# Kernel optimization log

Measured on AMD Instinct MI355X. Metric: run time of the kernel, lower is better.

## Reference

```python
import jax, jax.numpy as jnp
import numpy as np

SP = 4          # window/split size
HEADS = 8       # num_heads
SHIFTS = (0, 2) # shift_sizes


def _rel_pos_index(sp):
    # Same construction as the torch buffer `relative_position_index`.
    coords = np.stack(np.meshgrid(np.arange(sp), np.arange(sp), indexing='ij'))  # [2,sp,sp]
    coords = coords.reshape(2, -1)                                               # [2, sp*sp]
    rel = coords[:, :, None] - coords[:, None, :]                                # [2, N, N]
    rel = rel.transpose(1, 2, 0).astype(np.int64)                                # [N, N, 2]
    rel[..., 0] += sp - 1
    rel[..., 1] += sp - 1
    rel[..., 0] *= 2 * sp - 1
    return rel.sum(-1)  # [N, N]


def _window_attend(xh, qkv_w, lepe_w, bias, sp, heads, scale):
    # xh: [B, c, H, W] with c = split_dim
    B, c, H, W = xh.shape
    hd = c // heads
    h, w = H // sp, W // sp
    # 1x1 conv to qkv (no bias)
    qkv = jnp.einsum('oi,bihw->bohw', qkv_w, xh)
    q, k, v = jnp.split(qkv, 3, axis=1)
    # depthwise 3x3 LePE on v
    lepe = jax.lax.conv_general_dilated(v, lepe_w, (1, 1), 'SAME',
                                        feature_group_count=c)

    def part(t):
        # 'b (c head) (h hsp) (w wsp) -> (b h w) head (hsp wsp) c'
        t = t.reshape(B, hd, heads, h, sp, w, sp)
        t = t.transpose(0, 3, 5, 2, 4, 6, 1)  # b,h,w,head,hsp,wsp,hd
        return t.reshape(B * h * w, heads, sp * sp, hd)

    q, k, v, lepe = map(part, (q, k, v, lepe))
    attn = jnp.einsum('nhqc,nhkc->nhqk', q * scale, k) + bias[None]  # [N,heads,16,16]
    attn = jax.nn.softmax(attn, axis=-1)
    out = jnp.einsum('nhqk,nhkc->nhqc', attn, v) + lepe
    # inverse rearrange back to [B, c, H, W]
    out = out.reshape(B, h, w, heads, sp, sp, hd)
    out = out.transpose(0, 6, 3, 1, 4, 2, 5).reshape(B, c, H, W)
    return out


def setup_inputs() -> dict:
    key = jax.random.key(0)
    k1, k2, k3, k4 = jax.random.split(key, 4)
    x = jax.random.normal(k1, (8, 128, 192, 192), dtype=jnp.float32)
    qkv_w = jax.random.normal(k2, (192, 64), dtype=jnp.float32) * 0.05   # [3*split_dim, split_dim]
    lepe_w = jax.random.normal(k3, (64, 1, 3, 3), dtype=jnp.float32) * 0.05  # depthwise
    bias_table = jax.random.normal(k4, (49, 8), dtype=jnp.float32) * 0.02    # [(2sp-1)^2, heads]
    return {'x': x, 'qkv_w': qkv_w, 'lepe_w': lepe_w, 'bias_table': bias_table}


def reference(x, qkv_w, lepe_w, bias_table):
    B, C, H, W = x.shape
    c = C // 2
    hd = c // HEADS
    scale = hd ** -0.5
    idx = _rel_pos_index(SP)  # static numpy [16,16]
    bias = bias_table[idx.reshape(-1)].reshape(SP * SP, SP * SP, HEADS)
    bias = bias.transpose(2, 0, 1)  # [heads, 16, 16]

    results = []
    for s in SHIFTS:
        # NOTE: faithful to source, roll is over dims (1,2) = (channel, height)
        xs = jnp.roll(x, (-s, -s), axis=(1, 2)) if s > 0 else x
        halves = (xs[:, :c], xs[:, c:])
        outs = [_window_attend(xh, qkv_w, lepe_w, bias, SP, HEADS, scale)
                for xh in halves]
        if s > 0:
            outs = [jnp.roll(o, (s, s), axis=(1, 2)) for o in outs]
        results.append(jnp.concatenate(outs, axis=1))
    return results[0] + results[1]
```

## Files before the change

### kernel.cpp

```cpp
#include <hip/hip_runtime.h>

typedef __attribute__((ext_vector_type(8))) short short8v;
typedef __attribute__((ext_vector_type(8))) __fp16 h8v;
typedef __attribute__((ext_vector_type(2))) __fp16 h2v;
typedef __attribute__((ext_vector_type(4))) float f32x4;

__device__ inline unsigned short f2bf(float f) {
    unsigned u = __builtin_bit_cast(unsigned, f);
    return (unsigned short)((u + 0x7FFFu + ((u >> 16) & 1u)) >> 16);
}

__device__ inline float dot2(h2v a, h2v b, float c) {
#if __has_builtin(__builtin_amdgcn_fdot2)
    return __builtin_amdgcn_fdot2(a, b, c, false);
#else
    return c + (float)a[0] * (float)b[0] + (float)a[1] * (float)b[1];
#endif
}
__device__ inline h2v pk2h(float a, float b) {
#if __has_builtin(__builtin_amdgcn_cvt_pkrtz)
    return __builtin_bit_cast(h2v, __builtin_amdgcn_cvt_pkrtz(a, b));
#else
    h2v r; r[0] = (__fp16)a; r[1] = (__fp16)b; return r;
#endif
}
__device__ inline float fexp2(float x) {
#if __has_builtin(__builtin_amdgcn_exp2f)
    return __builtin_amdgcn_exp2f(x);
#else
    return __expf(x * 0.6931471805599453f);
#endif
}

__global__ __launch_bounds__(256) void prep_weights(const float* __restrict__ qkv_w,
                                                    __fp16* __restrict__ wf) {
    int it = blockIdx.x * 256 + threadIdx.x;
    if (it >= 1536) return;
    int l = it & 63, frag = it >> 6;
    int which = frag >> 3, nt = (frag >> 1) & 3, kst = frag & 1;
    const float* src = qkv_w + (which * 64 + nt * 16 + (l & 15)) * 64 + kst * 32 + (l >> 4) * 8;
    h8v pk;
    #pragma unroll
    for (int j = 0; j < 8; ++j) pk[j] = (__fp16)src[j];
    *reinterpret_cast<h8v*>(wf + it * 8) = pk;
}

__global__ __launch_bounds__(256) void prep_x(const float* __restrict__ x,
                                              __fp16* __restrict__ xh) {
    const int xt = blockIdx.x;
    const int y  = blockIdx.y;
    const int b  = blockIdx.z;
    const int x0 = xt * 32;
    __shared__ float buf[128 * 33];

    for (int it = threadIdx.x; it < 1024; it += 256) {
        int c = it >> 3, xq = it & 7;
        const float4 v = *reinterpret_cast<const float4*>(
            x + ((b * 128 + c) * 192 + y) * 192 + x0 + xq * 4);
        float* d = &buf[c * 33 + xq * 4];
        d[0] = v.x; d[1] = v.y; d[2] = v.z; d[3] = v.w;
    }
    __syncthreads();

    for (int it = threadIdx.x; it < 512; it += 256) {
        int xl = it >> 4, c8 = it & 15;
        int half = c8 >> 3, co = (c8 & 7) * 8;
        h8v pk;
        #pragma unroll
        for (int j = 0; j < 8; ++j) pk[j] = (__fp16)buf[(half * 64 + co + j) * 33 + xl];
        *reinterpret_cast<h8v*>(
            xh + (((size_t)((half * 8 + b) * 192 + y) * 192) + x0 + xl) * 64 + co) = pk;
    }
}

template<int SHIFT, bool ACCUM>
__global__ __launch_bounds__(256) void swin_main(
    const __fp16* __restrict__ xh,
    const __fp16* __restrict__ wfrag,
    const float* __restrict__ lepe_w,
    const float* __restrict__ bias_table,
    float* __restrict__ out)
{
    const int bx = blockIdx.x;
    const int wy = bx / 12, strip = bx % 12;
    const int half = blockIdx.y, b = blockIdx.z;
    const int tid = threadIdx.x;
    const int w = tid >> 6, l = tid & 63;

    __shared__ __fp16 pool[9216];
    __shared__ __fp16 qs[64 * 64];
    __shared__ __fp16 ks[64 * 64];
    __shared__ float  bias_s[392];
    __shared__ __fp16 lepe_s[576];

    for (int i = tid; i < 392; i += 256) bias_s[i] = bias_table[i] * 1.4426950408889634f;
    for (int i = tid; i < 576; i += 256) {
        int d = i & 7, rest = i >> 3;
        int j = rest % 9, h = rest / 9;
        lepe_s[i] = (__fp16)lepe_w[(d * 8 + h) * 9 + j];
    }

    const int ry0 = wy * 4 - 1, rx0 = strip * 16 - 1;
    for (int it = tid; it < 864; it += 256) {
        const int pos = it >> 3, slot = it & 7;
        const int py = pos / 18, px = pos - py * 18;
        const int ry = ry0 + py, rx = rx0 + px;
        h8v val;
        #pragma unroll
        for (int j = 0; j < 8; ++j) val[j] = (__fp16)0.f;
        if (ry >= 0 && ry < 192 && rx >= 0 && rx < 192) {
            int phys = ry + SHIFT; if (phys >= 192) phys -= 192;
            const int srcslot = slot ^ (pos & 7);
            const __fp16* base = xh + (((size_t)((half * 8 + b) * 192 + phys) * 192) + rx) * 64;
            if constexpr (SHIFT == 0) {
                val = *reinterpret_cast<const h8v*>(base + srcslot * 8);
            } else {
                int4 A = *reinterpret_cast<const int4*>(base + srcslot * 8);
                const int bchan = (half * 64 + srcslot * 8 + 8) & 127;
                const __fp16* bbase = xh +
                    (((size_t)(((bchan >> 6) * 8 + b) * 192 + phys) * 192) + rx) * 64;
                int B = *reinterpret_cast<const int*>(bbase + (bchan & 63));
                int4 R; R.x = A.y; R.y = A.z; R.z = A.w; R.w = B;
                val = __builtin_bit_cast(h8v, R);
            }
        }
        *reinterpret_cast<h8v*>(&pool[pos * 64 + slot * 8]) = val;
    }
    __syncthreads();

    const int tok16 = l & 15, g = l >> 4;
    h8v Aq[2], Av[3][2];
    {
        const int posq = (1 + (tok16 >> 2)) * 18 + w * 4 + 1 + (tok16 & 3);
        #pragma unroll
        for (int kst = 0; kst < 2; ++kst) {
            int chunk = (kst * 4 + g) ^ (posq & 7);
            Aq[kst] = *reinterpret_cast<const h8v*>(&pool[posq * 64 + chunk * 8]);
        }
        #pragma unroll
        for (int mt = 0; mt < 3; ++mt) {
            int t = mt * 16 + tok16;
            int posv = (t < 36) ? ((t / 6) * 18 + w * 4 + (t % 6)) : 0;
            #pragma unroll
            for (int kst = 0; kst < 2; ++kst) {
                int chunk = (kst * 4 + g) ^ (posv & 7);
                Av[mt][kst] = *reinterpret_cast<const h8v*>(&pool[posv * 64 + chunk * 8]);
            }
        }
    }
    __syncthreads();

    #pragma unroll
    for (int nt = 0; nt < 4; ++nt) {
        h8v Bq[2], Bk[2], Bv[2];
        #pragma unroll
        for (int kst = 0; kst < 2; ++kst) {
            Bq[kst] = *reinterpret_cast<const h8v*>(wfrag + (((0 * 8 + nt * 2 + kst) * 64 + l) * 8));
            Bk[kst] = *reinterpret_cast<const h8v*>(wfrag + (((1 * 8 + nt * 2 + kst) * 64 + l) * 8));
            Bv[kst] = *reinterpret_cast<const h8v*>(wfrag + (((2 * 8 + nt * 2 + kst) * 64 + l) * 8));
        }
        f32x4 aQ = {0.f,0.f,0.f,0.f}, aK = {0.f,0.f,0.f,0.f};
        f32x4 aV[3];
        #pragma unroll
        for (int mt = 0; mt < 3; ++mt) aV[mt] = (f32x4){0.f,0.f,0.f,0.f};
        #pragma unroll
        for (int kst = 0; kst < 2; ++kst) {
            aQ = __builtin_amdgcn_mfma_f32_16x16x32_f16(Aq[kst], Bq[kst], aQ, 0, 0, 0);
            aK = __builtin_amdgcn_mfma_f32_16x16x32_f16(Aq[kst], Bk[kst], aK, 0, 0, 0);
            #pragma unroll
            for (int mt = 0; mt < 3; ++mt)
                aV[mt] = __builtin_amdgcn_mfma_f32_16x16x32_f16(Av[mt][kst], Bv[kst], aV[mt], 0, 0, 0);
        }
        const int ch  = nt * 16 + tok16;
        const int chp = (ch & 7) * 8 + (ch >> 3);
        #pragma unroll
        for (int r = 0; r < 4; ++r) {
            const int qtok = w * 16 + 4 * g + r;
            const int pb = (((chp >> 3) ^ (qtok & 7)) * 8 + (chp & 7));
            qs[qtok * 64 + pb] = (__fp16)(aQ[r] * 0.5101293f);
            ks[qtok * 64 + pb] = (__fp16)aK[r];
        }
        #pragma unroll
        for (int mt = 0; mt < 3; ++mt)
            #pragma unroll
            for (int r = 0; r < 4; ++r) {
                const int t = mt * 16 + 4 * g + r;
                if (t < 36) {
                    const int pb = (((chp >> 3) ^ (t & 7)) * 8 + (chp & 7));
                    pool[(w * 36 + t) * 64 + pb] = (__fp16)aV[mt][r];
                }
            }
    }
    __syncthreads();

    {
        const int h = l >> 3, tqp = l & 7;
        const int qy0 = tqp >> 2, qx0 = tqp & 3;
        const __fp16* vv = &pool[w * 36 * 64];

        const int ox = strip * 16 + w * 4 + qx0;
        int oy0 = wy * 4 + qy0 + SHIFT;     if (oy0 >= 192) oy0 -= 192;
        int oy1 = wy * 4 + qy0 + 2 + SHIFT; if (oy1 >= 192) oy1 -= 192;
        const int ddelta = (oy1 - oy0) * 192;
        int idx0[8];
        float prev0[8], prev1[8];
        #pragma unroll
        for (int d = 0; d < 8; ++d) {
            const int oc = half * 64 + ((d * 8 + h + SHIFT) & 63);
            idx0[d] = ((b * 128 + oc) * 192 + oy0) * 192 + ox;
            if (ACCUM) { prev0[d] = out[idx0[d]]; prev1[d] = out[idx0[d] + ddelta]; }
        }

        const int t0 = w * 16 + tqp, t1 = t0 + 8;
        h8v q0 = *reinterpret_cast<const h8v*>(&qs[t0 * 64 + (h ^ (t0 & 7)) * 8]);
        h8v q1 = *reinterpret_cast<const h8v*>(&qs[t1 * 64 + (h ^ (t1 & 7)) * 8]);
        const h2v* q0p = reinterpret_cast<const h2v*>(&q0);
        const h2v* q1p = reinterpret_cast<const h2v*>(&q1);

        h2v scp0[8], scp1[8];
        float den0 = 0.f, den1 = 0.f;
        #pragma unroll
        for (int tkp = 0; tkp < 8; ++tkp) {
            float e0[2], e1[2];
            #pragma unroll
            for (int u = 0; u < 2; ++u) {
                const int tk = tkp * 2 + u;
                const int kt = w * 16 + tk;
                h8v kr = *reinterpret_cast<const h8v*>(&ks[kt * 64 + (h ^ (kt & 7)) * 8]);
                const h2v* kp = reinterpret_cast<const h2v*>(&kr);
                float s0 = 0.f, s1 = 0.f;
                #pragma unroll
                for (int i = 0; i < 4; ++i) { s0 = dot2(q0p[i], kp[i], s0); s1 = dot2(q1p[i], kp[i], s1); }
                const int ky = tk >> 2, kx = tk & 3;
                s0 += bias_s[((qy0 - ky + 3) * 7 + (qx0 - kx + 3)) * 8 + h];
                s1 += bias_s[((qy0 + 2 - ky + 3) * 7 + (qx0 - kx + 3)) * 8 + h];
                e0[u] = fexp2(s0); e1[u] = fexp2(s1);
            }
            den0 += e0[0] + e0[1]; den1 += e1[0] + e1[1];
            scp0[tkp] = pk2h(e0[0], e0[1]);
            scp1[tkp] = pk2h(e1[0], e1[1]);
        }
        const float inv0 = 1.f / den0, inv1 = 1.f / den1;
        const h2v ip0 = pk2h(inv0, inv0), ip1 = pk2h(inv1, inv1);

        h2v o0pk[4], o1pk[4];
        #pragma unroll
        for (int j = 0; j < 4; ++j) { o0pk[j] = pk2h(0.f, 0.f); o1pk[j] = pk2h(0.f, 0.f); }
        #pragma unroll
        for (int tkp = 0; tkp < 8; ++tkp) {
            const h2v w0 = scp0[tkp] * ip0;
            const h2v w1 = scp1[tkp] * ip1;
            #pragma unroll
            for (int u = 0; u < 2; ++u) {
                const int tk = tkp * 2 + u;
                const int t = (1 + (tk >> 2)) * 6 + 1 + (tk & 3);
                h8v vr = *reinterpret_cast<const h8v*>(&vv[t * 64 + (h ^ (t & 7)) * 8]);
                const h2v* vp = reinterpret_cast<const h2v*>(&vr);
                h2v b0; b0[0] = w0[u]; b0[1] = w0[u];
                h2v b1; b1[0] = w1[u]; b1[1] = w1[u];
                #pragma unroll
                for (int j = 0; j < 4; ++j) {
                    o0pk[j] += b0 * vp[j];
                    o1pk[j] += b1 * vp[j];
                }
            }
        }

        #pragma unroll
        for (int dy = 0; dy < 3; ++dy)
            #pragma unroll
            for (int dx = 0; dx < 3; ++dx) {
                const int ta = (qy0 + dy) * 6 + qx0 + dx;
                const int tb = ta + 12;
                h8v v0 = *reinterpret_cast<const h8v*>(&vv[ta * 64 + (h ^ (ta & 7)) * 8]);
                h8v v1 = *reinterpret_cast<const h8v*>(&vv[tb * 64 + (h ^ (tb & 7)) * 8]);
                h8v lw = *reinterpret_cast<const h8v*>(&lepe_s[(h * 9 + dy * 3 + dx) * 8]);
                const h2v* v0p = reinterpret_cast<const h2v*>(&v0);
                const h2v* v1p = reinterpret_cast<const h2v*>(&v1);
                const h2v* lwp = reinterpret_cast<const h2v*>(&lw);
                #pragma unroll
                for (int j = 0; j < 4; ++j) {
                    o0pk[j] += v0p[j] * lwp[j];
                    o1pk[j] += v1p[j] * lwp[j];
                }
            }

        #pragma unroll
        for (int d = 0; d < 8; ++d) {
            const float a0 = (float)o0pk[d >> 1][d & 1];
            const float a1 = (float)o1pk[d >> 1][d & 1];
            if (ACCUM) { out[idx0[d]] = prev0[d] + a0; out[idx0[d] + ddelta] = prev1[d] + a1; }
            else       { out[idx0[d]] = a0;            out[idx0[d] + ddelta] = a1; }
        }
    }
}

template<int SHIFT, bool ACCUM>
__global__ __launch_bounds__(256) void swin_fb(
    const float* __restrict__ x, const float* __restrict__ qkv_w,
    const float* __restrict__ lepe_w, const float* __restrict__ bias_table,
    float* __restrict__ out)
{
    const int C = 128, HH = 192, WW = 192;
    const int win = blockIdx.x, wy = win / 48, wx = win % 48;
    const int half = blockIdx.y, b = blockIdx.z, tid = threadIdx.x;
    __shared__ short xpA[8 * 64 * 8];
    __shared__ float vs[64 * 37], qsf[64 * 17], ksf[64 * 17];
    __shared__ float bias_s[392], lepe_s[576];
    const int ys0 = wy * 4, xs0 = wx * 4;
    for (int i = tid; i < 392; i += 256) bias_s[i] = bias_table[i];
    for (int i = tid; i < 576; i += 256) lepe_s[i] = lepe_w[i];
    for (int item = tid; item < 512; item += 256) {
        const int slot = item >> 6, l = item & 63, kst = slot & 1;
        int p = 0; bool tvalid = true;
        if (slot < 6) { int t48 = (slot >> 1) * 16 + (l & 15); tvalid = (t48 < 36); p = t48; }
        else { int ti = l & 15; p = (1 + (ti >> 2)) * 6 + 1 + (ti & 3); }
        const int c0 = kst * 32 + (l >> 4) * 8;
        short8v pk;
        #pragma unroll
        for (int j = 0; j < 8; ++j) pk[j] = 0;
        if (tvalid) {
            int py = p / 6, px = p - py * 6;
            int ry = ys0 - 1 + py, rx = xs0 - 1 + px;
            if (ry >= 0 && ry < HH && rx >= 0 && rx < WW) {
                int oy = ry + SHIFT; if (oy >= HH) oy -= HH;
                #pragma unroll
                for (int j = 0; j < 8; ++j) {
                    int oc = half * 64 + c0 + j + SHIFT; if (oc >= C) oc -= C;
                    pk[j] = (short)f2bf(x[((b * C + oc) * HH + oy) * WW + rx]);
                }
            }
        }
        *reinterpret_cast<short8v*>(&xpA[item * 8]) = pk;
    }
    const int w = tid >> 6, l = tid & 63, nn = l & 15, g = l >> 4;
    short8v Bq[2], Bk[2], Bv[2];
    #pragma unroll
    for (int kst = 0; kst < 2; ++kst) {
        const int coff = kst * 32 + g * 8;
        const float* s0 = qkv_w + (w * 16 + nn) * 64 + coff;
        const float* s1 = qkv_w + (64 + w * 16 + nn) * 64 + coff;
        const float* s2 = qkv_w + (128 + w * 16 + nn) * 64 + coff;
        short8v p0, p1, p2;
        #pragma unroll
        for (int j = 0; j < 8; ++j) { p0[j] = (short)f2bf(s0[j]); p1[j] = (short)f2bf(s1[j]); p2[j] = (short)f2bf(s2[j]); }
        Bq[kst] = p0; Bk[kst] = p1; Bv[kst] = p2;
    }
    __syncthreads();
    {
        short8v Aq[2], Avf[3][2];
        #pragma unroll
        for (int kst = 0; kst < 2; ++kst)
            Aq[kst] = *reinterpret_cast<const short8v*>(&xpA[((6 + kst) * 64 + l) * 8]);
        #pragma unroll
        for (int mt = 0; mt < 3; ++mt)
            #pragma unroll
            for (int kst = 0; kst < 2; ++kst)
                Avf[mt][kst] = *reinterpret_cast<const short8v*>(&xpA[((mt * 2 + kst) * 64 + l) * 8]);
        f32x4 aQ = {0,0,0,0}, aK = {0,0,0,0}; f32x4 aV[3];
        #pragma unroll
        for (int mt = 0; mt < 3; ++mt) aV[mt] = (f32x4){0,0,0,0};
        #pragma unroll
        for (int kst = 0; kst < 2; ++kst) {
            aQ = __builtin_amdgcn_mfma_f32_16x16x32_bf16(Aq[kst], Bq[kst], aQ, 0, 0, 0);
            aK = __builtin_amdgcn_mfma_f32_16x16x32_bf16(Aq[kst], Bk[kst], aK, 0, 0, 0);
            #pragma unroll
            for (int mt = 0; mt < 3; ++mt)
                aV[mt] = __builtin_amdgcn_mfma_f32_16x16x32_bf16(Avf[mt][kst], Bv[kst], aV[mt], 0, 0, 0);
        }
        const int ch = w * 16 + nn;
        #pragma unroll
        for (int r = 0; r < 4; ++r) { qsf[ch * 17 + g * 4 + r] = aQ[r]; ksf[ch * 17 + g * 4 + r] = aK[r]; }
        #pragma unroll
        for (int mt = 0; mt < 3; ++mt)
            #pragma unroll
            for (int r = 0; r < 4; ++r) { int tok = mt * 16 + g * 4 + r; if (tok < 36) vs[ch * 37 + tok] = aV[mt][r]; }
    }
    __syncthreads();
    {
        const int tq = tid & 15, h = (tid >> 4) & 7, dh = tid >> 7;
        const int qy = tq >> 2, qx = tq & 3;
        const float scale = 0.35355339059327373f;
        float qreg[8];
        #pragma unroll
        for (int d = 0; d < 8; ++d) qreg[d] = qsf[(d * 8 + h) * 17 + tq] * scale;
        float sc[16]; float m = -1e30f;
        #pragma unroll
        for (int tk = 0; tk < 16; ++tk) {
            float s = 0.f;
            #pragma unroll
            for (int d = 0; d < 8; ++d) s += qreg[d] * ksf[(d * 8 + h) * 17 + tk];
            s += bias_s[((qy - (tk >> 2) + 3) * 7 + (qx - (tk & 3) + 3)) * 8 + h];
            sc[tk] = s; m = fmaxf(m, s);
        }
        float den = 0.f;
        #pragma unroll
        for (int tk = 0; tk < 16; ++tk) { sc[tk] = __expf(sc[tk] - m); den += sc[tk]; }
        const float inv = 1.f / den;
        float lw[4][9];
        #pragma unroll
        for (int dd = 0; dd < 4; ++dd) {
            int ch = (dh * 4 + dd) * 8 + h;
            #pragma unroll
            for (int j = 0; j < 9; ++j) lw[dd][j] = lepe_s[ch * 9 + j];
        }
        float o[4] = {0,0,0,0};
        #pragma unroll
        for (int tk = 0; tk < 16; ++tk) {
            int p = (1 + (tk >> 2)) * 6 + 1 + (tk & 3); float s = sc[tk];
            #pragma unroll
            for (int dd = 0; dd < 4; ++dd) o[dd] += s * vs[((dh * 4 + dd) * 8 + h) * 37 + p];
        }
        int oy = ys0 + qy + SHIFT; if (oy >= HH) oy -= HH;
        const int irx = xs0 + qx;
        #pragma unroll
        for (int dd = 0; dd < 4; ++dd) {
            const int ch = (dh * 4 + dd) * 8 + h;
            float val = o[dd] * inv;
            #pragma unroll
            for (int dy = 0; dy < 3; ++dy)
                #pragma unroll
                for (int dx = 0; dx < 3; ++dx)
                    val += vs[ch * 37 + (qy + dy) * 6 + (qx + dx)] * lw[dd][dy * 3 + dx];
            const int oc = half * 64 + ((ch + SHIFT) & 63);
            const int oidx = ((b * C + oc) * HH + oy) * WW + irx;
            if (ACCUM) out[oidx] += val; else out[oidx] = val;
        }
    }
}

extern "C" void kernel_launch(void* const* d_in, const int* in_sizes, int n_in,
                              void* d_out, int out_size, void* d_ws, size_t ws_size,
                              hipStream_t stream) {
    const float* x          = (const float*)d_in[0];
    const float* qkv_w      = (const float*)d_in[1];
    const float* lepe_w     = (const float*)d_in[2];
    const float* bias_table = (const float*)d_in[3];
    float* out = (float*)d_out;

    const size_t XH_BYTES = 16UL * 192 * 192 * 64 * 2;
    const size_t NEED = 32768 + XH_BYTES;

    if (ws_size >= NEED) {
        __fp16* wf = (__fp16*)d_ws;
        __fp16* xh = (__fp16*)((char*)d_ws + 32768);
        prep_weights<<<6, 256, 0, stream>>>(qkv_w, wf);
        prep_x<<<dim3(6, 192, 8), 256, 0, stream>>>(x, xh);
        dim3 grid(576, 2, 8);
        swin_main<0, false><<<grid, 256, 0, stream>>>(xh, wf, lepe_w, bias_table, out);
        swin_main<2, true ><<<grid, 256, 0, stream>>>(xh, wf, lepe_w, bias_table, out);
    } else {
        dim3 grid(48 * 48, 2, 8);
        swin_fb<0, false><<<grid, 256, 0, stream>>>(x, qkv_w, lepe_w, bias_table, out);
        swin_fb<2, true ><<<grid, 256, 0, stream>>>(x, qkv_w, lepe_w, bias_table, out);
    }
}
```

Measured before the change: 323.5 us.

## Stage first-shift result in fp16 scratch buffer and bit-reverse head-dim channel order

The first shift pass now writes its partial output to an fp16 workspace buffer instead of the fp32 output. The second pass reads that buffer and writes the final fp32 sum, which removes one full fp32 read and one fp32 write of the output tensor. The per-head channel positions in the shared-memory q/k/v layouts and the LePE weights are also permuted with a 3-bit reversal, changing which output channels each lane stores in sequence, likely to improve store coalescing. The cost is fp16 rounding of the intermediate partial sum and extra workspace.

New measurement: 336.4 us. 1.04x slower.

```diff
diff --git a/kernel.cpp b/kernel.cpp
--- a/kernel.cpp
+++ b/kernel.cpp
@@ -9,7 +9,6 @@
     unsigned u = __builtin_bit_cast(unsigned, f);
     return (unsigned short)((u + 0x7FFFu + ((u >> 16) & 1u)) >> 16);
 }
-
 __device__ inline float dot2(h2v a, h2v b, float c) {
 #if __has_builtin(__builtin_amdgcn_fdot2)
     return __builtin_amdgcn_fdot2(a, b, c, false);
@@ -30,6 +29,9 @@
 #else
     return __expf(x * 0.6931471805599453f);
 #endif
+}
+__device__ __host__ inline int rev3(int x) {
+    return ((x & 1) << 2) | (x & 2) | ((x >> 2) & 1);
 }
 
 __global__ __launch_bounds__(256) void prep_weights(const float* __restrict__ qkv_w,
@@ -73,13 +75,14 @@
     }
 }
 
-template<int SHIFT, bool ACCUM>
+template<int SHIFT, int MODE>
 __global__ __launch_bounds__(256) void swin_main(
     const __fp16* __restrict__ xh,
     const __fp16* __restrict__ wfrag,
     const float* __restrict__ lepe_w,
     const float* __restrict__ bias_table,
-    float* __restrict__ out)
+    float* __restrict__ out,
+    __fp16* __restrict__ pbuf)
 {
     const int bx = blockIdx.x;
     const int wy = bx / 12, strip = bx % 12;
@@ -95,9 +98,10 @@
 
     for (int i = tid; i < 392; i += 256) bias_s[i] = bias_table[i] * 1.4426950408889634f;
     for (int i = tid; i < 576; i += 256) {
-        int d = i & 7, rest = i >> 3;
+        int pos = i & 7, rest = i >> 3;
         int j = rest % 9, h = rest / 9;
-        lepe_s[i] = (__fp16)lepe_w[(d * 8 + h) * 9 + j];
+        int d = rev3(pos);
+        lepe_s[i] = (__fp16)lepe_w[(8 * d + h) * 9 + j];
     }
 
     const int ry0 = wy * 4 - 1, rx0 = strip * 16 - 1;
@@ -171,12 +175,13 @@
             for (int mt = 0; mt < 3; ++mt)
                 aV[mt] = __builtin_amdgcn_mfma_f32_16x16x32_f16(Av[mt][kst], Bv[kst], aV[mt], 0, 0, 0);
         }
-        const int ch  = nt * 16 + tok16;
-        const int chp = (ch & 7) * 8 + (ch >> 3);
+        const int ch    = nt * 16 + tok16;
+        const int hpart = ch & 7;
+        const int e     = rev3(ch >> 3);
         #pragma unroll
         for (int r = 0; r < 4; ++r) {
             const int qtok = w * 16 + 4 * g + r;
-            const int pb = (((chp >> 3) ^ (qtok & 7)) * 8 + (chp & 7));
+            const int pb = ((hpart ^ (qtok & 7)) << 3) + e;
             qs[qtok * 64 + pb] = (__fp16)(aQ[r] * 0.5101293f);
             ks[qtok * 64 + pb] = (__fp16)aK[r];
         }
@@ -186,7 +191,7 @@
             for (int r = 0; r < 4; ++r) {
                 const int t = mt * 16 + 4 * g + r;
                 if (t < 36) {
-                    const int pb = (((chp >> 3) ^ (t & 7)) * 8 + (chp & 7));
+                    const int pb = ((hpart ^ (t & 7)) << 3) + e;
                     pool[(w * 36 + t) * 64 + pb] = (__fp16)aV[mt][r];
                 }
             }
@@ -205,10 +210,15 @@
         int idx0[8];
         float prev0[8], prev1[8];
         #pragma unroll
-        for (int d = 0; d < 8; ++d) {
+        for (int pos = 0; pos < 8; ++pos) {
+            const int d = rev3(pos);
             const int oc = half * 64 + ((d * 8 + h + SHIFT) & 63);
-            idx0[d] = ((b * 128 + oc) * 192 + oy0) * 192 + ox;
-            if (ACCUM) { prev0[d] = out[idx0[d]]; prev1[d] = out[idx0[d] + ddelta]; }
+            idx0[pos] = ((b * 128 + oc) * 192 + oy0) * 192 + ox;
+            if constexpr (MODE == 1) {
+                prev0[pos] = out[idx0[pos]]; prev1[pos] = out[idx0[pos] + ddelta];
+            } else if constexpr (MODE == 3) {
+                prev0[pos] = (float)pbuf[idx0[pos]]; prev1[pos] = (float)pbuf[idx0[pos] + ddelta];
+            }
         }
 
         const int t0 = w * 16 + tqp, t1 = t0 + 8;
@@ -286,11 +296,16 @@
             }
 
         #pragma unroll
-        for (int d = 0; d < 8; ++d) {
-            const float a0 = (float)o0pk[d >> 1][d & 1];
-            const float a1 = (float)o1pk[d >> 1][d & 1];
-            if (ACCUM) { out[idx0[d]] = prev0[d] + a0; out[idx0[d] + ddelta] = prev1[d] + a1; }
-            else       { out[idx0[d]] = a0;            out[idx0[d] + ddelta] = a1; }
+        for (int pos = 0; pos < 8; ++pos) {
+            const float a0 = (float)o0pk[pos >> 1][pos & 1];
+            const float a1 = (float)o1pk[pos >> 1][pos & 1];
+            if constexpr (MODE == 0) {
+                out[idx0[pos]] = a0;                 out[idx0[pos] + ddelta] = a1;
+            } else if constexpr (MODE == 2) {
+                pbuf[idx0[pos]] = (__fp16)a0;        pbuf[idx0[pos] + ddelta] = (__fp16)a1;
+            } else {
+                out[idx0[pos]] = prev0[pos] + a0;    out[idx0[pos] + ddelta] = prev1[pos] + a1;
+            }
         }
     }
 }
@@ -439,7 +454,9 @@
     float* out = (float*)d_out;
 
     const size_t XH_BYTES = 16UL * 192 * 192 * 64 * 2;
-    const size_t NEED = 32768 + XH_BYTES;
+    const size_t PB_BYTES = 8UL * 128 * 192 * 192 * 2;
+    const size_t NEED  = 32768 + XH_BYTES;
+    const size_t NEED2 = NEED + PB_BYTES;
 
     if (ws_size >= NEED) {
         __fp16* wf = (__fp16*)d_ws;
@@ -447,8 +464,14 @@
         prep_weights<<<6, 256, 0, stream>>>(qkv_w, wf);
         prep_x<<<dim3(6, 192, 8), 256, 0, stream>>>(x, xh);
         dim3 grid(576, 2, 8);
-        swin_main<0, false><<<grid, 256, 0, stream>>>(xh, wf, lepe_w, bias_table, out);
-        swin_main<2, true ><<<grid, 256, 0, stream>>>(xh, wf, lepe_w, bias_table, out);
+        if (ws_size >= NEED2) {
+            __fp16* pbuf = (__fp16*)((char*)d_ws + NEED);
+            swin_main<0, 2><<<grid, 256, 0, stream>>>(xh, wf, lepe_w, bias_table, out, pbuf);
+            swin_main<2, 3><<<grid, 256, 0, stream>>>(xh, wf, lepe_w, bias_table, out, pbuf);
+        } else {
+            swin_main<0, 0><<<grid, 256, 0, stream>>>(xh, wf, lepe_w, bias_table, out, nullptr);
+            swin_main<2, 1><<<grid, 256, 0, stream>>>(xh, wf, lepe_w, bias_table, out, nullptr);
+        }
     } else {
         dim3 grid(48 * 48, 2, 8);
         swin_fb<0, false><<<grid, 256, 0, stream>>>(x, qkv_w, lepe_w, bias_table, out);
```
